# Kernel tuning notes

Measured on AMD Instinct MI355X. Metric: run time of the kernel, lower is better.

Reference implementation:

```python
import jax, jax.numpy as jnp
import numpy as np

B, NPG, DEG = 256, 128, 16          # graphs per side, nodes per graph, avg degree
N = B * NPG                          # 32768 nodes per side
E = N * DEG                          # 524288 edges per side
F_IN, F1, F2, F3 = 64, 128, 64, 32   # number_labels, filters_1..3
TN, BINS = 16, 16                    # tensor_neurons, bins


def setup_inputs() -> dict:
    key = jax.random.key(0)
    ks = jax.random.split(key, 24)

    def make_edges(k):
        # random edges, each constrained within its own graph block
        base = jax.random.randint(k, (2, E), 0, NPG)
        off = jnp.repeat(jnp.arange(B, dtype=jnp.int64) * NPG, NPG * DEG)
        return (base + off[None, :]).astype(jnp.int64)

    def w(k, shape, fan_in):
        return (jax.random.normal(k, shape, jnp.float32) / np.sqrt(fan_in)).astype(jnp.float32)

    batch = jnp.repeat(jnp.arange(B, dtype=jnp.int64), NPG)
    return {
        'x1': jax.random.normal(ks[0], (N, F_IN), jnp.float32),
        'edge_index_1': make_edges(ks[1]),
        'batch_1': batch,
        'x2': jax.random.normal(ks[2], (N, F_IN), jnp.float32),
        'edge_index_2': make_edges(ks[3]),
        'batch_2': batch,
        # GCN layer params
        'W1': w(ks[4], (F_IN, F1), F_IN), 'b1': jnp.zeros((F1,), jnp.float32),
        'W2': w(ks[5], (F1, F2), F1),     'b2': jnp.zeros((F2,), jnp.float32),
        'W3': w(ks[6], (F2, F3), F2),     'b3': jnp.zeros((F3,), jnp.float32),
        # attention pooling
        'attW': w(ks[7], (F3, F3), F3),
        # tensor network module
        'tW': w(ks[8], (F3, F3, TN), F3),
        'tblock': w(ks[9], (TN, 2 * F3), 2 * F3),
        'tbias': jnp.zeros((TN,), jnp.float32),
        # scoring MLP (feature_count = TN + BINS -> 16 -> 1)
        'sW1': w(ks[10], (TN + BINS, 16), TN + BINS), 'sb1': jnp.zeros((16,), jnp.float32),
        'sW2': w(ks[11], (16, 1), 16),                'sb2': jnp.zeros((1,), jnp.float32),
    }


def _gcn(x, W, b, src, dst):
    # PyG GCNConv: add self-loops, symmetric deg^-1/2 normalization, then scatter-add
    n = x.shape[0]
    loop = jnp.arange(n, dtype=src.dtype)
    s = jnp.concatenate([src, loop])
    d = jnp.concatenate([dst, loop])
    deg = jax.ops.segment_sum(jnp.ones_like(d, dtype=x.dtype), d, num_segments=n)
    dinv = jax.lax.rsqrt(jnp.maximum(deg, 1e-12))
    norm = dinv[s] * dinv[d]                      # [E+N]
    h = x @ W                                     # [N, Fout]
    out = jax.ops.segment_sum(norm[:, None] * h[s], d, num_segments=n)
    return out + b


def _histc(v):
    # torch.histc with bins=BINS, min=max=0 -> uses data min/max; last bin inclusive
    v = v.reshape(-1)
    lo, hi = v.min(), v.max()
    idx = jnp.floor((v - lo) / jnp.maximum(hi - lo, 1e-12) * BINS)
    idx = jnp.clip(idx, 0, BINS - 1).astype(jnp.int32)
    h = jax.ops.segment_sum(jnp.ones_like(v), idx, num_segments=BINS)
    return h / h.sum()


def reference(x1, edge_index_1, batch_1, x2, edge_index_2, batch_2,
              W1, b1, W2, b2, W3, b3, attW, tW, tblock, tbias,
              sW1, sb1, sW2, sb2):
    def conv_pass(x, ei):
        src, dst = ei[0], ei[1]
        h = jax.nn.relu(_gcn(x, W1, b1, src, dst))   # dropout inactive (eval)
        h = jax.nn.relu(_gcn(h, W2, b2, src, dst))
        return _gcn(h, W3, b3, src, dst)

    f1 = conv_pass(x1, edge_index_1)
    f2 = conv_pass(x2, edge_index_2)

    # to_dense_batch: equal-sized, batch-sorted graphs -> plain reshape, full masks
    d1 = f1.reshape(B, NPG, F3)
    d2 = f2.reshape(B, NPG, F3)

    # per-graph-pair similarity histogram (detached in original)
    scores = jnp.einsum('bnd,bmd->bnm', jax.lax.stop_gradient(d1), jax.lax.stop_gradient(d2))
    hist = jax.vmap(_histc)(jax.nn.sigmoid(scores))  # [B, BINS]

    # attention pooling (SimGNN AttentionModule)
    def attn_pool(d):
        ctx = jnp.tanh(jnp.mean(d @ attW, axis=1))             # [B, F3]
        att = jax.nn.sigmoid(jnp.einsum('bnd,bd->bn', d, ctx))  # [B, NPG]
        return jnp.einsum('bnd,bn->bd', d, att)                 # [B, F3]

    e1 = attn_pool(d1)
    e2 = attn_pool(d2)

    # tensor network scoring
    tensor_scores = jnp.einsum('bi,ijk,bj->bk', e1, tW, e2)
    block_scores = jnp.concatenate([e1, e2], axis=-1) @ tblock.T
    tnm = jax.nn.relu(tensor_scores + block_scores + tbias)      # [B, TN]

    feat = jnp.concatenate([tnm, hist], axis=1)                  # [B, TN+BINS]
    h = jax.nn.relu(feat @ sW1 + sb1)
    score = jax.nn.sigmoid(h @ sW2 + sb2)
    return score.squeeze(-1)                                     # [B]
```

## Files before the change

### kernel.cpp

```cpp
#include <hip/hip_runtime.h>
#include <hip/hip_bf16.h>
#include <hip/hip_fp16.h>

#define N_NODES 32768
#define N_EDGES 524288
#define NGRAPH  256
#define NPG     128
#define EPG     2048
#define F_IN    64
#define F1      128
#define F2      64
#define F3      32
#define TN      16
#define BINS    16

typedef _Float16 f16;
typedef _Float16 f16x4 __attribute__((ext_vector_type(4)));
typedef _Float16 f16x8 __attribute__((ext_vector_type(8)));
typedef float    f32x4 __attribute__((ext_vector_type(4)));

__device__ __forceinline__ float sigmoidf(float x) { return 1.f / (1.f + expf(-x)); }

#define L_A    0
#define L_R1   34816
#define L_R2   69632
#define L_R3   88064
#define L_R4   106496
#define L_R5   123904
#define L_DT   128512
#define L_DINV 148992
#define POOLB  149504

#define SA  136
#define SB  72
#define SD  40
#define LHS 1040

template<int N, int K, int AS, int BS, int OS, bool TRANS, bool RELU>
__device__ __forceinline__ void mfma_mm(const f16* __restrict__ A,
                                        const f16* __restrict__ B,
                                        const float* __restrict__ bias,
                                        f16* __restrict__ out, int tid) {
    const int w = tid >> 6, lane = tid & 63;
    const int col = lane & 15, g = lane >> 4;
    const int strip = w & 7, nh = w >> 3;
    const int rowa = strip * 16 + col;
    constexpr int NT = N / 16, KS = K / 32, NT2 = NT / 2;
    f32x4 acc[NT2];
#pragma unroll
    for (int nt = 0; nt < NT2; ++nt) {
        const float b = bias ? bias[(nh * NT2 + nt) * 16 + col] : 0.f;
        acc[nt] = (f32x4){b, b, b, b};
    }
#pragma unroll
    for (int ks = 0; ks < KS; ++ks) {
        const f16x8 a = *(const f16x8*)&A[rowa * AS + ks * 32 + g * 8];
#pragma unroll
        for (int nt = 0; nt < NT2; ++nt) {
            const f16x8 b = *(const f16x8*)&B[((nh * NT2 + nt) * 16 + col) * BS + ks * 32 + g * 8];
            acc[nt] = __builtin_amdgcn_mfma_f32_16x16x32_f16(a, b, acc[nt], 0, 0, 0);
        }
    }
#pragma unroll
    for (int nt = 0; nt < NT2; ++nt) {
        const int c = (nh * NT2 + nt) * 16 + col;
        if (TRANS) {
            f16x4 o;
#pragma unroll
            for (int j = 0; j < 4; ++j) {
                float v = acc[nt][j];
                if (RELU) v = fmaxf(v, 0.f);
                o[j] = (f16)v;
            }
            *(f16x4*)&out[c * OS + strip * 16 + g * 4] = o;
        } else {
#pragma unroll
            for (int j = 0; j < 4; ++j) {
                float v = acc[nt][j];
                if (RELU) v = fmaxf(v, 0.f);
                out[(strip * 16 + g * 4 + j) * OS + c] = (f16)v;
            }
        }
    }
}

__global__ __launch_bounds__(1024, 4) void genn_all(
    const float* __restrict__ x1, const int* __restrict__ ei1,
    const float* __restrict__ x2, const int* __restrict__ ei2,
    const float* __restrict__ W1, const float* __restrict__ b1,
    const float* __restrict__ W2, const float* __restrict__ b2,
    const float* __restrict__ W3, const float* __restrict__ b3,
    const float* __restrict__ attW, const float* __restrict__ tW,
    const float* __restrict__ tblk, const float* __restrict__ tbias,
    const float* __restrict__ sW1, const float* __restrict__ sb1,
    const float* __restrict__ sW2, const float* __restrict__ sb2,
    float* __restrict__ outp) {
    __shared__ __align__(16) char pool[POOLB];
    unsigned int* Acnt = (unsigned int*)(pool + L_A);
    f16*   Amat = (f16*)(pool + L_A);
    f16*   dts  = (f16*)(pool + L_DT);
    float* dinv = (float*)(pool + L_DINV);

    const int g = blockIdx.x;
    const int tid = threadIdx.x;
    const int wv = tid >> 6, lane = tid & 63;

    for (int side = 0; side < 2; ++side) {
        const float* xg = (side ? x2 : x1) + (size_t)g * NPG * F_IN;
        const int* eib  = side ? ei2 : ei1;
        const int* srcg = eib + (size_t)g * EPG;
        const int* dstg = eib + N_EDGES + (size_t)g * EPG;
        const int nb = g * NPG;

        for (int i = tid; i < 2176; i += 1024)
            ((uint4*)Acnt)[i] = make_uint4(0, 0, 0, 0);
        __syncthreads();

#pragma unroll
        for (int it = 0; it < EPG / 1024; ++it) {
            const int e = it * 1024 + tid;
            const int d = dstg[e] - nb;
            const int s = srcg[e] - nb;
            atomicAdd(&Acnt[d * 68 + (s >> 1)], 1u << ((s & 1) << 4));
        }
        {
            f16* xT = (f16*)(pool + L_R1);
#pragma unroll
            for (int it = 0; it < 2; ++it) {
                const int idx = (it * 1024 + tid) * 4;
                const float4 v = *(const float4*)&xg[idx];
                const int n = idx >> 6, c = idx & 63;
                xT[(c + 0) * SA + n] = (f16)v.x;
                xT[(c + 1) * SA + n] = (f16)v.y;
                xT[(c + 2) * SA + n] = (f16)v.z;
                xT[(c + 3) * SA + n] = (f16)v.w;
            }
            if (side == 0) {
                f16* W1T = (f16*)(pool + L_R2);
                for (int i = tid; i < F_IN * F1; i += 1024)
                    W1T[(i & 127) * SB + (i >> 7)] = (f16)W1[i];
                f16* W2T = (f16*)(pool + L_R4);
                for (int i = tid; i < F1 * F2; i += 1024)
                    W2T[(i & 63) * SA + (i >> 6)] = (f16)W2[i];
                f16* W3T = (f16*)(pool + L_R5);
                for (int i = tid; i < F2 * F3; i += 1024)
                    W3T[(i & 31) * SB + (i >> 5)] = (f16)W3[i];
            }
        }
        __syncthreads();

        if (tid < 512) {
            const int d = tid >> 2, q = tid & 3;
            unsigned int s = 0;
            const unsigned int* rp = &Acnt[d * 68 + q * 17];
            for (int j = 0; j < 17; ++j) {
                const unsigned int v = rp[j];
                s += (v & 0xffffu) + (v >> 16);
            }
            s += __shfl_down((int)s, 2);
            s += __shfl_down((int)s, 1);
            if (q == 0) dinv[d] = rsqrtf((float)s + 1.0f);
        }
        __syncthreads();

        for (int i = tid; i < 8704; i += 1024) {
            const int d = i / 68, w = i % 68;
            const unsigned int v = Acnt[i];
            const int s0 = 2 * w, s1 = 2 * w + 1;
            int c0 = v & 0xffffu, c1 = v >> 16;
            if (s0 == d) ++c0;
            if (s1 == d) ++c1;
            const float dd = dinv[d];
            const f16 f0 = (f16)((float)c0 * dinv[s0 & 127] * dd);
            const f16 f1 = (f16)((float)c1 * dinv[s1 & 127] * dd);
            unsigned short u0 = __builtin_bit_cast(unsigned short, f0);
            unsigned short u1 = __builtin_bit_cast(unsigned short, f1);
            Acnt[i] = (unsigned int)u0 | ((unsigned int)u1 << 16);
        }
        __syncthreads();

        f16* xT   = (f16*)(pool + L_R1);
        f16* h1   = (f16*)(pool + L_R1);
        f16* h2   = (f16*)(pool + L_R1);
        f16* W1T  = (f16*)(pool + L_R2);
        f16* out1 = (f16*)(pool + L_R3);
        f16* t2T  = (f16*)(pool + L_R3);
        f16* t3T  = (f16*)(pool + L_R3);
        f16* W2T  = (f16*)(pool + L_R4);
        f16* W3T  = (f16*)(pool + L_R5);

        mfma_mm<64, 128, SA, SA, SB, false, false>(Amat, xT, nullptr, out1, tid);
        __syncthreads();
        mfma_mm<128, 64, SB, SB, SA, false, true>(out1, W1T, b1, h1, tid);
        __syncthreads();
        mfma_mm<64, 128, SA, SA, SA, true, false>(h1, W2T, nullptr, t2T, tid);
        __syncthreads();
        mfma_mm<64, 128, SA, SA, SB, false, true>(Amat, t2T, b2, h2, tid);
        __syncthreads();
        mfma_mm<32, 64, SB, SB, SA, true, false>(h2, W3T, nullptr, t3T, tid);
        __syncthreads();
        mfma_mm<32, 128, SA, SA, SD, false, false>(Amat, t3T, b3,
                                                   dts + side * (NPG * SD), tid);
        __syncthreads();
    }

    unsigned char* lhist = (unsigned char*)(pool + L_R4);
    float* pf   = (float*)(pool + L_R3);
    float* red  = pf;
    float* lohi = pf + 32;
    float* meanv= pf + 34;
    float* ctxv = pf + 98;
    float* ev   = pf + 162;
    float* feat = pf + 226;
    float* hv   = pf + 258;
    float* av   = pf + 290;
    float* pmean= pf + 546;
    float* ptens= pf + 1570;
    int*   bins2= (int*)(pf + 2082);
    const f16* d1 = dts;
    const f16* d2 = dts + NPG * SD;

    const int col = lane & 15, gq = lane >> 4;
    const int strip = wv & 7, nh = wv >> 3;
    const int rowa = strip * 16 + col;
    f32x4 acc[4];
#pragma unroll
    for (int nt = 0; nt < 4; ++nt) acc[nt] = (f32x4){0.f, 0.f, 0.f, 0.f};
    {
        const f16x8 a = *(const f16x8*)&d1[rowa * SD + gq * 8];
#pragma unroll
        for (int nt = 0; nt < 4; ++nt) {
            const f16x8 b = *(const f16x8*)&d2[((nh * 4 + nt) * 16 + col) * SD + gq * 8];
            acc[nt] = __builtin_amdgcn_mfma_f32_16x16x32_f16(a, b, acc[nt], 0, 0, 0);
        }
    }
    for (int i = tid; i < 17 * LHS / 4; i += 1024) ((unsigned int*)lhist)[i] = 0u;
    float lmin = acc[0][0], lmax = acc[0][0];
#pragma unroll
    for (int nt = 0; nt < 4; ++nt)
#pragma unroll
        for (int j = 0; j < 4; ++j) {
            lmin = fminf(lmin, acc[nt][j]);
            lmax = fmaxf(lmax, acc[nt][j]);
        }
    for (int off = 32; off; off >>= 1) {
        lmin = fminf(lmin, __shfl_down(lmin, off));
        lmax = fmaxf(lmax, __shfl_down(lmax, off));
    }
    if (lane == 0) { red[wv] = lmin; red[16 + wv] = lmax; }
    __syncthreads();
    if (tid == 0) {
        float mn = red[0], mx = red[16];
        for (int w = 1; w < 16; ++w) { mn = fminf(mn, red[w]); mx = fmaxf(mx, red[16 + w]); }
        const float los = sigmoidf(mn);
        const float den = fmaxf(sigmoidf(mx) - los, 1e-12f);
        lohi[0] = los;
        lohi[1] = (float)BINS / den;
    }
    __syncthreads();

    {
        const float lo = lohi[0], sc = lohi[1];
        unsigned char* lh = lhist + tid;
#pragma unroll
        for (int nt = 0; nt < 4; ++nt)
#pragma unroll
            for (int j = 0; j < 4; ++j) {
                const float v = sigmoidf(acc[nt][j]);
                int b = (int)((v - lo) * sc);
                b = min(max(b, 0), BINS - 1);
                lh[b * LHS]++;
            }
    }
    __syncthreads();
    if (tid < 256) {
        const int b = tid & 15, chunk = tid >> 4;
        const unsigned char* row = lhist + b * LHS + chunk * 64;
        int s = 0;
#pragma unroll
        for (int i = 0; i < 4; ++i) {
            const uint4 v = *(const uint4*)(row + i * 16);
            unsigned int u;
            u = v.x; s += (u & 255) + ((u >> 8) & 255) + ((u >> 16) & 255) + (u >> 24);
            u = v.y; s += (u & 255) + ((u >> 8) & 255) + ((u >> 16) & 255) + (u >> 24);
            u = v.z; s += (u & 255) + ((u >> 8) & 255) + ((u >> 16) & 255) + (u >> 24);
            u = v.w; s += (u & 255) + ((u >> 8) & 255) + ((u >> 16) & 255) + (u >> 24);
        }
        bins2[chunk * 16 + b] = s;
    }
    __syncthreads();

    {
        const int cc = tid & 63, chunk = tid >> 6;
        const int side = cc >> 5, c = cc & 31;
        const f16* dp = dts + side * (NPG * SD);
        float s = 0.f;
        const int nbs = chunk * 8;
        for (int n = 0; n < 8; ++n) s += (float)dp[(nbs + n) * SD + c];
        pmean[chunk * 64 + cc] = s;
    }
    __syncthreads();
    if (tid < 64) {
        float s = 0.f;
        for (int c = 0; c < 16; ++c) s += pmean[c * 64 + tid];
        meanv[tid] = s * (1.f / NPG);
    }
    __syncthreads();
    if (tid < 64) {
        const int c = tid & 31;
        const float* mv = &meanv[(tid >> 5) * 32];
        float a = 0.f;
        for (int k = 0; k < F3; ++k) a += mv[k] * attW[k * F3 + c];
        ctxv[tid] = tanhf(a);
    }
    __syncthreads();
    if (tid < 256) {
        const int n = tid & 127, side = tid >> 7;
        const f16* dp = dts + side * (NPG * SD);
        const float* cx = &ctxv[side * 32];
        float a = 0.f;
        for (int k = 0; k < F3; ++k) a += (float)dp[n * SD + k] * cx[k];
        av[tid] = sigmoidf(a);
    }
    __syncthreads();
    {
        const int cc = tid & 63, chunk = tid >> 6;
        const int side = cc >> 5, c = cc & 31;
        const f16* dp = dts + side * (NPG * SD);
        const float* a = &av[side * 128];
        float s = 0.f;
        const int nbs = chunk * 8;
        for (int n = 0; n < 8; ++n) s += a[nbs + n] * (float)dp[(nbs + n) * SD + c];
        pmean[chunk * 64 + cc] = s;
    }
    __syncthreads();
    if (tid < 64) {
        float s = 0.f;
        for (int c = 0; c < 16; ++c) s += pmean[c * 64 + tid];
        ev[tid] = s;
    }
    __syncthreads();

    if (tid < 512) {
        const int k = tid & 15, i = tid >> 4;
        const float e1i = ev[i];
        float a = 0.f;
        for (int j = 0; j < F3; ++j) a += ev[32 + j] * tW[(i * F3 + j) * TN + k];
        ptens[i * 16 + k] = e1i * a;
    }
    __syncthreads();
    if (tid < TN) {
        float a = tbias[tid];
        for (int i = 0; i < 32; ++i) a += ptens[i * 16 + tid];
        for (int i = 0; i < F3; ++i) a += ev[i] * tblk[tid * 2 * F3 + i];
        for (int j = 0; j < F3; ++j) a += ev[32 + j] * tblk[tid * 2 * F3 + F3 + j];
        feat[tid] = fmaxf(a, 0.f);
    } else if (tid < TN + BINS) {
        const int b = tid - TN;
        int s = 0;
        for (int c = 0; c < 16; ++c) s += bins2[c * 16 + b];
        feat[tid] = (float)s * (1.f / (NPG * NPG));
    }
    __syncthreads();
    if (tid < 16) {
        float a = sb1[tid];
        for (int i = 0; i < TN + BINS; ++i) a += feat[i] * sW1[i * 16 + tid];
        hv[tid] = fmaxf(a, 0.f);
    }
    __syncthreads();
    if (tid == 0) {
        float a = sb2[0];
        for (int j = 0; j < 16; ++j) a += hv[j] * sW2[j];
        outp[g] = sigmoidf(a);
    }
}

extern "C" void kernel_launch(void* const* d_in, const int* in_sizes, int n_in,
                              void* d_out, int out_size, void* d_ws, size_t ws_size,
                              hipStream_t stream) {
    const float* x1   = (const float*)d_in[0];
    const int*   ei1  = (const int*)d_in[1];
    const float* x2   = (const float*)d_in[3];
    const int*   ei2  = (const int*)d_in[4];
    const float* W1   = (const float*)d_in[6];
    const float* b1   = (const float*)d_in[7];
    const float* W2   = (const float*)d_in[8];
    const float* b2   = (const float*)d_in[9];
    const float* W3   = (const float*)d_in[10];
    const float* b3   = (const float*)d_in[11];
    const float* attW = (const float*)d_in[12];
    const float* tW   = (const float*)d_in[13];
    const float* tblk = (const float*)d_in[14];
    const float* tbias= (const float*)d_in[15];
    const float* sW1  = (const float*)d_in[16];
    const float* sb1  = (const float*)d_in[17];
    const float* sW2  = (const float*)d_in[18];
    const float* sb2  = (const float*)d_in[19];
    float* out = (float*)d_out;
    (void)in_sizes; (void)n_in; (void)out_size; (void)d_ws; (void)ws_size;

    genn_all<<<NGRAPH, 1024, 0, stream>>>(x1, ei1, x2, ei2,
                                          W1, b1, W2, b2, W3, b3,
                                          attW, tW, tblk, tbias,
                                          sW1, sb1, sW2, sb2, out);
}
```

Measured before the change: 33.29 us.

## Count both sides' edges up front using packed 4-bit counters for side two

Unrolls the two-side loop and builds the side-two adjacency counts at the start, packed as 4-bit counters in spare shared memory alongside the side-one 16-bit counts. Both degree reductions run in one phase split across thread halves. The side-two x loads are issued before its normalization pass, so the global latency overlaps LDS work, and several barriers and zero-fill passes are dropped. The cost is that 4-bit counters overflow if any (dst,src) pair appears 16 or more times, which random edges make unlikely but not impossible.

```diff
diff --git a/kernel.cpp b/kernel.cpp
--- a/kernel.cpp
+++ b/kernel.cpp
@@ -100,109 +100,177 @@
     f16*   Amat = (f16*)(pool + L_A);
     f16*   dts  = (f16*)(pool + L_DT);
     float* dinv = (float*)(pool + L_DINV);
+    unsigned int* cnt4  = (unsigned int*)(pool + L_DT + 10240);
+    float*        dinvB = (float*)(pool + L_DT + 18432);
 
     const int g = blockIdx.x;
     const int tid = threadIdx.x;
     const int wv = tid >> 6, lane = tid & 63;
-
-    for (int side = 0; side < 2; ++side) {
-        const float* xg = (side ? x2 : x1) + (size_t)g * NPG * F_IN;
-        const int* eib  = side ? ei2 : ei1;
-        const int* srcg = eib + (size_t)g * EPG;
-        const int* dstg = eib + N_EDGES + (size_t)g * EPG;
-        const int nb = g * NPG;
-
-        for (int i = tid; i < 2176; i += 1024)
-            ((uint4*)Acnt)[i] = make_uint4(0, 0, 0, 0);
-        __syncthreads();
-
-#pragma unroll
-        for (int it = 0; it < EPG / 1024; ++it) {
-            const int e = it * 1024 + tid;
-            const int d = dstg[e] - nb;
-            const int s = srcg[e] - nb;
-            atomicAdd(&Acnt[d * 68 + (s >> 1)], 1u << ((s & 1) << 4));
-        }
-        {
-            f16* xT = (f16*)(pool + L_R1);
-#pragma unroll
-            for (int it = 0; it < 2; ++it) {
-                const int idx = (it * 1024 + tid) * 4;
-                const float4 v = *(const float4*)&xg[idx];
-                const int n = idx >> 6, c = idx & 63;
-                xT[(c + 0) * SA + n] = (f16)v.x;
-                xT[(c + 1) * SA + n] = (f16)v.y;
-                xT[(c + 2) * SA + n] = (f16)v.z;
-                xT[(c + 3) * SA + n] = (f16)v.w;
-            }
-            if (side == 0) {
-                f16* W1T = (f16*)(pool + L_R2);
-                for (int i = tid; i < F_IN * F1; i += 1024)
-                    W1T[(i & 127) * SB + (i >> 7)] = (f16)W1[i];
-                f16* W2T = (f16*)(pool + L_R4);
-                for (int i = tid; i < F1 * F2; i += 1024)
-                    W2T[(i & 63) * SA + (i >> 6)] = (f16)W2[i];
-                f16* W3T = (f16*)(pool + L_R5);
-                for (int i = tid; i < F2 * F3; i += 1024)
-                    W3T[(i & 31) * SB + (i >> 5)] = (f16)W3[i];
-            }
-        }
-        __syncthreads();
-
-        if (tid < 512) {
-            const int d = tid >> 2, q = tid & 3;
-            unsigned int s = 0;
-            const unsigned int* rp = &Acnt[d * 68 + q * 17];
-            for (int j = 0; j < 17; ++j) {
-                const unsigned int v = rp[j];
-                s += (v & 0xffffu) + (v >> 16);
-            }
-            s += __shfl_down((int)s, 2);
-            s += __shfl_down((int)s, 1);
-            if (q == 0) dinv[d] = rsqrtf((float)s + 1.0f);
-        }
-        __syncthreads();
-
-        for (int i = tid; i < 8704; i += 1024) {
-            const int d = i / 68, w = i % 68;
-            const unsigned int v = Acnt[i];
-            const int s0 = 2 * w, s1 = 2 * w + 1;
-            int c0 = v & 0xffffu, c1 = v >> 16;
-            if (s0 == d) ++c0;
-            if (s1 == d) ++c1;
-            const float dd = dinv[d];
-            const f16 f0 = (f16)((float)c0 * dinv[s0 & 127] * dd);
-            const f16 f1 = (f16)((float)c1 * dinv[s1 & 127] * dd);
+    const int nb = g * NPG;
+
+    for (int i = tid; i < 2176; i += 1024)
+        ((uint4*)Acnt)[i] = make_uint4(0, 0, 0, 0);
+    if (tid < 512) ((uint4*)cnt4)[tid] = make_uint4(0, 0, 0, 0);
+    __syncthreads();
+
+#pragma unroll
+    for (int it = 0; it < 2; ++it) {
+        const int e = it * 1024 + tid;
+        const int d = ei1[N_EDGES + (size_t)g * EPG + e] - nb;
+        const int s = ei1[(size_t)g * EPG + e] - nb;
+        atomicAdd(&Acnt[d * 68 + (s >> 1)], 1u << ((s & 1) << 4));
+    }
+#pragma unroll
+    for (int it = 0; it < 2; ++it) {
+        const int e = it * 1024 + tid;
+        const int d = ei2[N_EDGES + (size_t)g * EPG + e] - nb;
+        const int s = ei2[(size_t)g * EPG + e] - nb;
+        atomicAdd(&cnt4[d * 16 + (s >> 3)], 1u << ((s & 7) << 2));
+    }
+    {
+        const float* xg = x1 + (size_t)g * NPG * F_IN;
+        f16* xT = (f16*)(pool + L_R1);
+#pragma unroll
+        for (int it = 0; it < 2; ++it) {
+            const int idx = (it * 1024 + tid) * 4;
+            const float4 v = *(const float4*)&xg[idx];
+            const int n = idx >> 6, c = idx & 63;
+            xT[(c + 0) * SA + n] = (f16)v.x;
+            xT[(c + 1) * SA + n] = (f16)v.y;
+            xT[(c + 2) * SA + n] = (f16)v.z;
+            xT[(c + 3) * SA + n] = (f16)v.w;
+        }
+        f16* W1T = (f16*)(pool + L_R2);
+        for (int i = tid; i < F_IN * F1; i += 1024)
+            W1T[(i & 127) * SB + (i >> 7)] = (f16)W1[i];
+        f16* W2T = (f16*)(pool + L_R4);
+        for (int i = tid; i < F1 * F2; i += 1024)
+            W2T[(i & 63) * SA + (i >> 6)] = (f16)W2[i];
+        f16* W3T = (f16*)(pool + L_R5);
+        for (int i = tid; i < F2 * F3; i += 1024)
+            W3T[(i & 31) * SB + (i >> 5)] = (f16)W3[i];
+    }
+    __syncthreads();
+
+    if (tid < 512) {
+        const int d = tid >> 2, q = tid & 3;
+        unsigned int s = 0;
+        const unsigned int* rp = &Acnt[d * 68 + q * 17];
+        for (int j = 0; j < 17; ++j) {
+            const unsigned int v = rp[j];
+            s += (v & 0xffffu) + (v >> 16);
+        }
+        s += __shfl_down((int)s, 2);
+        s += __shfl_down((int)s, 1);
+        if (q == 0) dinv[d] = rsqrtf((float)s + 1.0f);
+    } else {
+        const int t = tid - 512;
+        const int d = t >> 2, q = t & 3;
+        unsigned int s = 0;
+#pragma unroll
+        for (int k = 0; k < 4; ++k) {
+            const unsigned int v = cnt4[d * 16 + q * 4 + k];
+            const unsigned int v2 = (v & 0x0F0F0F0Fu) + ((v >> 4) & 0x0F0F0F0Fu);
+            s += (v2 & 0xFFu) + ((v2 >> 8) & 0xFFu) + ((v2 >> 16) & 0xFFu) + (v2 >> 24);
+        }
+        s += __shfl_down((int)s, 2);
+        s += __shfl_down((int)s, 1);
+        if (q == 0) dinvB[d] = rsqrtf((float)s + 1.0f);
+    }
+    __syncthreads();
+
+    for (int i = tid; i < 8704; i += 1024) {
+        const int d = i / 68, w = i % 68;
+        const unsigned int v = Acnt[i];
+        const int s0 = 2 * w, s1 = 2 * w + 1;
+        int c0 = v & 0xffffu, c1 = v >> 16;
+        if (s0 == d) ++c0;
+        if (s1 == d) ++c1;
+        const float dd = dinv[d];
+        const f16 f0 = (f16)((float)c0 * dinv[s0 & 127] * dd);
+        const f16 f1 = (f16)((float)c1 * dinv[s1 & 127] * dd);
+        unsigned short u0 = __builtin_bit_cast(unsigned short, f0);
+        unsigned short u1 = __builtin_bit_cast(unsigned short, f1);
+        Acnt[i] = (unsigned int)u0 | ((unsigned int)u1 << 16);
+    }
+    __syncthreads();
+
+    f16* xT   = (f16*)(pool + L_R1);
+    f16* h1   = (f16*)(pool + L_R1);
+    f16* h2   = (f16*)(pool + L_R1);
+    f16* W1T  = (f16*)(pool + L_R2);
+    f16* out1 = (f16*)(pool + L_R3);
+    f16* t2T  = (f16*)(pool + L_R3);
+    f16* t3T  = (f16*)(pool + L_R3);
+    f16* W2T  = (f16*)(pool + L_R4);
+    f16* W3T  = (f16*)(pool + L_R5);
+
+    mfma_mm<64, 128, SA, SA, SB, false, false>(Amat, xT, nullptr, out1, tid);
+    __syncthreads();
+    mfma_mm<128, 64, SB, SB, SA, false, true>(out1, W1T, b1, h1, tid);
+    __syncthreads();
+    mfma_mm<64, 128, SA, SA, SA, true, false>(h1, W2T, nullptr, t2T, tid);
+    __syncthreads();
+    mfma_mm<64, 128, SA, SA, SB, false, true>(Amat, t2T, b2, h2, tid);
+    __syncthreads();
+    mfma_mm<32, 64, SB, SB, SA, true, false>(h2, W3T, nullptr, t3T, tid);
+    __syncthreads();
+    mfma_mm<32, 128, SA, SA, SD, false, false>(Amat, t3T, b3, dts, tid);
+    __syncthreads();
+
+    {
+        const float* xg = x2 + (size_t)g * NPG * F_IN;
+        float4 xv0 = *(const float4*)&xg[tid * 4];
+        float4 xv1 = *(const float4*)&xg[(1024 + tid) * 4];
+        const int d = tid >> 3, q = tid & 7;
+        const float dd = dinvB[d];
+#pragma unroll
+        for (int k = 0; k < 8; ++k) {
+            const int w = q + k * 8;
+            const int c0 = 2 * w;
+            const unsigned int vin = cnt4[d * 16 + (c0 >> 3)];
+            const int sh = (c0 & 7) << 2;
+            int n0 = (vin >> sh) & 15;
+            int n1 = (vin >> (sh + 4)) & 15;
+            if (c0 == d) ++n0;
+            if (c0 + 1 == d) ++n1;
+            const f16 f0 = (f16)((float)n0 * dinvB[c0] * dd);
+            const f16 f1 = (f16)((float)n1 * dinvB[c0 + 1] * dd);
             unsigned short u0 = __builtin_bit_cast(unsigned short, f0);
             unsigned short u1 = __builtin_bit_cast(unsigned short, f1);
-            Acnt[i] = (unsigned int)u0 | ((unsigned int)u1 << 16);
-        }
-        __syncthreads();
-
-        f16* xT   = (f16*)(pool + L_R1);
-        f16* h1   = (f16*)(pool + L_R1);
-        f16* h2   = (f16*)(pool + L_R1);
-        f16* W1T  = (f16*)(pool + L_R2);
-        f16* out1 = (f16*)(pool + L_R3);
-        f16* t2T  = (f16*)(pool + L_R3);
-        f16* t3T  = (f16*)(pool + L_R3);
-        f16* W2T  = (f16*)(pool + L_R4);
-        f16* W3T  = (f16*)(pool + L_R5);
-
-        mfma_mm<64, 128, SA, SA, SB, false, false>(Amat, xT, nullptr, out1, tid);
-        __syncthreads();
-        mfma_mm<128, 64, SB, SB, SA, false, true>(out1, W1T, b1, h1, tid);
-        __syncthreads();
-        mfma_mm<64, 128, SA, SA, SA, true, false>(h1, W2T, nullptr, t2T, tid);
-        __syncthreads();
-        mfma_mm<64, 128, SA, SA, SB, false, true>(Amat, t2T, b2, h2, tid);
-        __syncthreads();
-        mfma_mm<32, 64, SB, SB, SA, true, false>(h2, W3T, nullptr, t3T, tid);
-        __syncthreads();
-        mfma_mm<32, 128, SA, SA, SD, false, false>(Amat, t3T, b3,
-                                                   dts + side * (NPG * SD), tid);
-        __syncthreads();
-    }
+            Acnt[d * 68 + w] = (unsigned int)u0 | ((unsigned int)u1 << 16);
+        }
+        {
+            const int idx = tid * 4;
+            const int n = idx >> 6, c = idx & 63;
+            xT[(c + 0) * SA + n] = (f16)xv0.x;
+            xT[(c + 1) * SA + n] = (f16)xv0.y;
+            xT[(c + 2) * SA + n] = (f16)xv0.z;
+            xT[(c + 3) * SA + n] = (f16)xv0.w;
+        }
+        {
+            const int idx = (1024 + tid) * 4;
+            const int n = idx >> 6, c = idx & 63;
+            xT[(c + 0) * SA + n] = (f16)xv1.x;
+            xT[(c + 1) * SA + n] = (f16)xv1.y;
+            xT[(c + 2) * SA + n] = (f16)xv1.z;
+            xT[(c + 3) * SA + n] = (f16)xv1.w;
+        }
+    }
+    __syncthreads();
+
+    mfma_mm<64, 128, SA, SA, SB, false, false>(Amat, xT, nullptr, out1, tid);
+    __syncthreads();
+    mfma_mm<128, 64, SB, SB, SA, false, true>(out1, W1T, b1, h1, tid);
+    __syncthreads();
+    mfma_mm<64, 128, SA, SA, SA, true, false>(h1, W2T, nullptr, t2T, tid);
+    __syncthreads();
+    mfma_mm<64, 128, SA, SA, SB, false, true>(Amat, t2T, b2, h2, tid);
+    __syncthreads();
+    mfma_mm<32, 64, SB, SB, SA, true, false>(h2, W3T, nullptr, t3T, tid);
+    __syncthreads();
+    mfma_mm<32, 128, SA, SA, SD, false, false>(Amat, t3T, b3, dts + NPG * SD, tid);
+    __syncthreads();
 
     unsigned char* lhist = (unsigned char*)(pool + L_R4);
     float* pf   = (float*)(pool + L_R3);
```

Measured after the change: 32.09 us (median of 2 runs). -3.6%, faster.
